# Kernel optimization log

Hardware: AMD Instinct MI355X
Metric: run time of the kernel (lower is better)

The kernel has to match this reference:

```python
import jax, jax.numpy as jnp
import numpy as np

N, E, G, B = 50000, 1600000, 128, 128
FP = 33     # num_feature_pro
ED = 128    # embed_dim
ML = 3000   # max_len


def setup_inputs() -> dict:
    key = jax.random.key(0)
    ks = jax.random.split(key, 20)
    s = lambda k, shape: jax.random.normal(k, shape, jnp.float32) * 0.02
    inp = {}
    inp["pro_x"] = jax.random.normal(ks[0], (N, FP), jnp.float32)
    inp["edge_index"] = jax.random.randint(ks[1], (2, E), 0, N)
    inp["edge_weight"] = jax.random.uniform(ks[2], (E,), jnp.float32)
    inp["pro_batch"] = jnp.sort(jax.random.randint(ks[3], (N,), 0, G))
    inp["rna_global"] = jax.random.randint(ks[4], (B, ML), 0, 5)
    inp["rna_local"] = jax.random.randint(ks[5], (B, ML - 2), 0, 65)
    inp["emb1"] = s(ks[6], (5, ED))
    inp["emb2"] = s(ks[7], (65, ED))
    inp["convW1"] = s(ks[8], (32, ML, 8));     inp["convb1"] = jnp.zeros((32,), jnp.float32)
    inp["convW2"] = s(ks[9], (32, ML - 2, 8)); inp["convb2"] = jnp.zeros((32,), jnp.float32)
    inp["fcxr_W"] = s(ks[10], (32 * 121, 128)); inp["fcxr_b"] = jnp.zeros((128,), jnp.float32)
    inp["gcn1_W"] = s(ks[11], (FP, FP));         inp["gcn1_b"] = jnp.zeros((FP,), jnp.float32)
    inp["gcn2_W"] = s(ks[12], (FP, 2 * FP));     inp["gcn2_b"] = jnp.zeros((2 * FP,), jnp.float32)
    inp["gcn3_W"] = s(ks[13], (2 * FP, 4 * FP)); inp["gcn3_b"] = jnp.zeros((4 * FP,), jnp.float32)
    inp["bn1_g"] = jnp.ones((FP,), jnp.float32);     inp["bn1_b"] = jnp.zeros((FP,), jnp.float32)
    inp["bn2_g"] = jnp.ones((2 * FP,), jnp.float32); inp["bn2_b"] = jnp.zeros((2 * FP,), jnp.float32)
    inp["bn3_g"] = jnp.ones((4 * FP,), jnp.float32); inp["bn3_b"] = jnp.zeros((4 * FP,), jnp.float32)
    inp["fcg1_W"] = s(ks[14], (4 * FP, 1024)); inp["fcg1_b"] = jnp.zeros((1024,), jnp.float32)
    inp["fcg2_W"] = s(ks[15], (1024, 128));    inp["fcg2_b"] = jnp.zeros((128,), jnp.float32)
    return inp


def _gcn(x, W, b, src, dst, ew, n):
    # PyG GCNConv: x' = D^{-1/2}(A+I)D^{-1/2} (x W) + b, self-loop weight 1
    xw = x @ W                                           # [n, out]
    deg = jax.ops.segment_sum(ew, dst, num_segments=n) + 1.0
    dis = jax.lax.rsqrt(deg)
    norm = dis[src] * ew * dis[dst]                      # [E]
    out = jax.ops.segment_sum(xw[src] * norm[:, None], dst, num_segments=n)
    out = out + xw * (dis * dis)[:, None]                # self loops
    return out + b


def _bn(x, g, b, eps=1e-5):
    # NodeLevelBatchNorm (training): batch stats over the node dim, biased var
    m = x.mean(0)
    v = ((x - m) ** 2).mean(0)
    return (x - m) * jax.lax.rsqrt(v + eps) * g + b


def _conv1d(x, W, b):
    # x: [B, C, L], W: [O, C, K] -> [B, O, L-K+1]
    y = jax.lax.conv_general_dilated(x, W, (1,), 'VALID',
                                     dimension_numbers=('NCH', 'OIH', 'NCH'))
    return y + b[None, :, None]


def _rna(tok, emb, cW, cb, fW, fb):
    e = emb[tok]                     # [B, seq, 128] -> channels=seq, length=128
    y = _conv1d(e, cW, cb)           # [B, 32, 121]
    return y.reshape(y.shape[0], -1) @ fW + fb


def reference(pro_x, edge_index, edge_weight, pro_batch, rna_global, rna_local,
              emb1, emb2, convW1, convb1, convW2, convb2, fcxr_W, fcxr_b,
              gcn1_W, gcn1_b, gcn2_W, gcn2_b, gcn3_W, gcn3_b,
              bn1_g, bn1_b, bn2_g, bn2_b, bn3_g, bn3_b,
              fcg1_W, fcg1_b, fcg2_W, fcg2_b):
    src, dst = edge_index[0], edge_index[1]
    n = pro_x.shape[0]
    # RNA branch (fc_xr shared between global and local)
    xrg = _rna(rna_global, emb1, convW1, convb1, fcxr_W, fcxr_b)
    xrl = _rna(rna_local, emb2, convW2, convb2, fcxr_W, fcxr_b)
    # Protein GCN branch
    xp = jax.nn.relu(_bn(_gcn(pro_x, gcn1_W, gcn1_b, src, dst, edge_weight, n), bn1_g, bn1_b))
    ones = jnp.ones_like(edge_weight)
    xp = jax.nn.relu(_bn(_gcn(xp, gcn2_W, gcn2_b, src, dst, ones, n), bn2_g, bn2_b))
    xp = jax.nn.relu(_bn(_gcn(xp, gcn3_W, gcn3_b, src, dst, ones, n), bn3_g, bn3_b))
    # global mean pool per graph
    cnt = jax.ops.segment_sum(jnp.ones((n,), xp.dtype), pro_batch, num_segments=G)
    pooled = jax.ops.segment_sum(xp, pro_batch, num_segments=G) / jnp.maximum(cnt, 1.0)[:, None]
    h = jax.nn.relu(pooled @ fcg1_W + fcg1_b)
    xp_out = h @ fcg2_W + fcg2_b     # dropout = identity (eval)
    xc_rna = (xrg + xrl) * 0.5       # mean over stacked [xrg, xrl]
    return (xc_rna, xp_out)
```

## Files before the change

kernel.cpp:

```cpp
#include <hip/hip_runtime.h>
#include <hip/hip_bf16.h>

typedef __hip_bfloat16 bf16;
typedef unsigned short u16;

#define NN 50000
#define NE 1600000
#define NG 128
#define NB 128
#define SG 3000
#define SL 2998
#define VG 5
#define VL 65
#define EDB 6250
#define AGB 12500
#define NA  (NB*VG + NB*VL)
#define NGB (32*VG + 32*VL)
#define CASTB ((NN*40+255)/256)

__device__ __forceinline__ float b2f(bf16 x){ return __bfloat162float(x); }
__device__ __forceinline__ float blo(unsigned u){ return __uint_as_float(u << 16); }
__device__ __forceinline__ float bhi(unsigned u){ return __uint_as_float(u & 0xffff0000u); }

__device__ void dev_buildG(float (*rows)[128], const float* __restrict__ emb,
                           const float* __restrict__ W, bf16* __restrict__ G,
                           int V, int q){
    int o = q / V, mt = q - o*V;
    int t = threadIdx.x;
    int j = t & 127, half = t >> 7;
    int kk[4], vv[4];
    #pragma unroll
    for (int qq = 0; qq < 4; ++qq){
        int mm = half*4 + qq;
        int m = mt*8 + mm;
        int k = m / V, v = m - k*V;
        kk[qq] = k; vv[qq] = v;
        rows[mm][j] = emb[v*128 + j];
    }
    __syncthreads();
    float a0=0.f, a1=0.f, a2=0.f, a3=0.f;
    const float* Wo = W + o*121*128 + j;
    for (int l = 0; l < 121; ++l){
        float w = Wo[l*128];
        a0 += rows[half*4+0][l + kk[0]] * w;
        a1 += rows[half*4+1][l + kk[1]] * w;
        a2 += rows[half*4+2][l + kk[2]] * w;
        a3 += rows[half*4+3][l + kk[3]] * w;
    }
    float a[4] = {a0, a1, a2, a3};
    #pragma unroll
    for (int qq = 0; qq < 4; ++qq){
        int row = vv[qq]*256 + o*8 + kk[qq];
        G[(size_t)row*128 + j] = __float2bfloat16(a[qq]);
    }
}

__global__ void k_front(const int* __restrict__ rna_g, const int* __restrict__ rna_l,
                        int* __restrict__ tcnt_g, int* __restrict__ toff_g,
                        u16* __restrict__ bucket_g,
                        int* __restrict__ tcnt_l, int* __restrict__ toff_l,
                        u16* __restrict__ bucket_l,
                        const float* __restrict__ convW1, const float* __restrict__ convW2,
                        bf16* __restrict__ Wr1, bf16* __restrict__ Wr2,
                        const float* __restrict__ fcxrW, const float* __restrict__ cb1,
                        const float* __restrict__ cb2, float* __restrict__ bias0,
                        const int* __restrict__ dst, const float* __restrict__ ew,
                        double* __restrict__ packed, int* __restrict__ slot,
                        const float* __restrict__ emb1, const float* __restrict__ emb2,
                        bf16* __restrict__ G1, bf16* __restrict__ G2,
                        const float* __restrict__ pro_x, bf16* __restrict__ xb0){
    __shared__ int hist[VL], pre[VL], cur[VL];
    __shared__ float rows[8][128];
    int bx = blockIdx.x;
    int t = threadIdx.x;
    if (bx < 2*NB){
        int br = bx & 1, b = bx >> 1;
        const int* tok = br ? rna_l : rna_g;
        int S = br ? SL : SG, V = br ? VL : VG;
        int* tcnt = br ? tcnt_l : tcnt_g;
        int* toff = br ? toff_l : toff_g;
        u16* bucket = br ? bucket_l : bucket_g;
        if (t < V) hist[t] = 0;
        __syncthreads();
        for (int i = t; i < S; i += 256) atomicAdd(&hist[tok[b*S + i]], 1);
        __syncthreads();
        if (t == 0){
            int run = 0;
            for (int v = 0; v < V; ++v){ pre[v] = run; run += hist[v]; }
        }
        __syncthreads();
        if (t < V){
            tcnt[b*V + t] = hist[t];
            toff[b*V + t] = pre[t];
            cur[t] = pre[t];
        }
        __syncthreads();
        for (int i = t; i < S; i += 256){
            int v = tok[b*S + i];
            int p = atomicAdd(&cur[v], 1);
            bucket[b*S + p] = (u16)i;
        }
        return;
    }
    bx -= 2*NB;
    if (bx < NGB){
        if (bx < 32*VG) dev_buildG(rows, emb1, fcxrW, G1, VG, bx);
        else dev_buildG(rows, emb2, fcxrW, G2, VL, bx - 32*VG);
        return;
    }
    bx -= NGB;
    if (bx < EDB){
        int e = bx*256 + t;
        double old = unsafeAtomicAdd(&packed[dst[e]], 1048576.0 + (double)ew[e]);
        slot[e] = (int)(old * (1.0/1048576.0));
        return;
    }
    bx -= EDB;
    if (bx < SG + SL){
        const float* W; bf16* Wr; int S, c = bx;
        if (c < SG){ W = convW1; Wr = Wr1; S = SG; }
        else { c -= SG; W = convW2; Wr = Wr2; S = SL; }
        Wr[c*256 + t] = __float2bfloat16(W[((t >> 3)*S + c)*8 + (t & 7)]);
        return;
    }
    bx -= SG + SL;
    if (bx < CASTB){
        int i = bx*256 + t;
        if (i >= NN*40) return;
        int n = i / 40, f = i - n*40;
        xb0[i] = __float2bfloat16(f < 33 ? pro_x[n*33 + f] : 0.f);
        return;
    }
    bx -= CASTB;
    if (t >= 128) return;
    int o = bx, j = t;
    float s = 0.f;
    const float* Wo = fcxrW + o*121*128 + j;
    for (int l = 0; l < 121; ++l) s += Wo[l*128];
    unsafeAtomicAdd(&bias0[j], 0.5f * (cb1[o] + cb2[o]) * s);
}

__device__ void dev_buildA(const bf16* __restrict__ Wr, const u16* __restrict__ bucket,
                           const int* __restrict__ toff, const int* __restrict__ tcnt,
                           float* __restrict__ A, int S, int V, int bv){
    int b = bv / V, v = bv - b*V;
    int t = threadIdx.x;
    const u16* bk = bucket + b*S + toff[b*V + v];
    int m = tcnt[b*V + v];
    float acc = 0.f;
    int idx = 0;
    for (; idx + 4 <= m; idx += 4){
        int c0 = bk[idx], c1 = bk[idx+1], c2 = bk[idx+2], c3 = bk[idx+3];
        acc += b2f(Wr[c0*256 + t]);
        acc += b2f(Wr[c1*256 + t]);
        acc += b2f(Wr[c2*256 + t]);
        acc += b2f(Wr[c3*256 + t]);
    }
    for (; idx < m; ++idx) acc += b2f(Wr[bk[idx]*256 + t]);
    A[b*(256*V) + v*256 + t] = acc;
}

__global__ void k_prep(const double* __restrict__ packed, int* __restrict__ cnt,
                       float2* __restrict__ dis12, float2* __restrict__ self12,
                       const int* __restrict__ batch, int* __restrict__ gstart,
                       int* __restrict__ bsum,
                       const float* __restrict__ fcxrb, const float* __restrict__ bias0,
                       float* __restrict__ out0){
    __shared__ int sd[256];
    int t = threadIdx.x;
    if (blockIdx.x == 49){
        for (int idx = t; idx < NB*128; idx += 256)
            out0[idx] = fcxrb[idx & 127] + bias0[idx & 127];
        return;
    }
    int base = blockIdx.x*1024;
    int s = 0;
    #pragma unroll
    for (int j = 0; j < 4; ++j){
        int i = base + t*4 + j;
        if (i < NN){
            double p = packed[i];
            int c = (int)(p * (1.0/1048576.0));
            float w = (float)(p - (double)c * 1048576.0);
            cnt[i] = c; s += c;
            float r1 = rsqrtf(w + 1.0f);
            float r2 = rsqrtf((float)c + 1.0f);
            dis12[i] = make_float2(r1, r2);
            self12[i] = make_float2(r1*r1, r2*r2);
            int pb = batch[i];
            int prev = (i == 0) ? -1 : batch[i-1];
            for (int g = prev + 1; g <= pb; ++g) gstart[g] = i;
            if (i == NN - 1){
                for (int g = pb + 1; g <= NG; ++g) gstart[g] = NN;
            }
        }
    }
    sd[t] = s; __syncthreads();
    for (int d = 128; d > 0; d >>= 1){
        if (t < d) sd[t] += sd[t+d];
        __syncthreads();
    }
    if (t == 0) bsum[blockIdx.x] = sd[0];
}

__global__ void k_scan3(const int* __restrict__ cnt, const int* __restrict__ bsum,
                        int* __restrict__ offs){
    __shared__ int sd[256];
    __shared__ int sbase;
    int t = threadIdx.x;
    if (t == 0){
        int run = 0;
        for (int i = 0; i < blockIdx.x; ++i) run += bsum[i];
        sbase = run;
    }
    int base = blockIdx.x*1024;
    int loc[4]; int s = 0;
    #pragma unroll
    for (int j = 0; j < 4; ++j){
        int idx = base + t*4 + j;
        loc[j] = (idx < NN) ? cnt[idx] : 0;
        s += loc[j];
    }
    sd[t] = s; __syncthreads();
    for (int d = 1; d < 256; d <<= 1){
        int v = (t >= d) ? sd[t-d] : 0;
        __syncthreads();
        sd[t] += v;
        __syncthreads();
    }
    int run = sbase + (sd[t] - s);
    #pragma unroll
    for (int j = 0; j < 4; ++j){
        int idx = base + t*4 + j;
        if (idx < NN) offs[idx] = run;
        run += loc[j];
    }
}

__global__ void k_F2(const bf16* __restrict__ Wr1, const bf16* __restrict__ Wr2,
                     const u16* __restrict__ bucket_g, const int* __restrict__ toff_g,
                     const int* __restrict__ tcnt_g, float* __restrict__ Ag,
                     const u16* __restrict__ bucket_l, const int* __restrict__ toff_l,
                     const int* __restrict__ tcnt_l, float* __restrict__ Al,
                     const int* __restrict__ src, const int* __restrict__ dst,
                     const float* __restrict__ ew, const float2* __restrict__ dis12,
                     const int* __restrict__ offs, const int* __restrict__ slot,
                     float4* __restrict__ epk){
    int bx = blockIdx.x;
    if (bx < NA){
        if (bx < NB*VG) dev_buildA(Wr1, bucket_g, toff_g, tcnt_g, Ag, SG, VG, bx);
        else dev_buildA(Wr2, bucket_l, toff_l, tcnt_l, Al, SL, VL, bx - NB*VG);
        return;
    }
    int e = (bx - NA)*256 + threadIdx.x;
    int s = src[e], d = dst[e];
    int pos = offs[d] + slot[e];
    float2 a = dis12[s], b = dis12[d];
    float4 v;
    v.x = __int_as_float(s*80);
    v.y = a.x * ew[e] * b.x;
    v.z = a.y * b.y;
    v.w = __int_as_float(s*144);
    epk[pos] = v;
}

template<int QV, int GRP, int OFF_W, int N_Z>
__device__ void dev_agg(float* sAgg ,
                        const bf16* __restrict__ xb, const float4* __restrict__ epk,
                        const int* __restrict__ offs, const int* __restrict__ cnt,
                        const float2* __restrict__ self12,
                        const float* __restrict__ W, const float* __restrict__ bias,
                        float* __restrict__ tout, float* __restrict__ bnpart,
                        int F, int OF, int bx){
    const int LPG = 64 / GRP;
    int wave = threadIdx.x >> 6;
    int node = bx*4 + wave;
    int lane = threadIdx.x & 63;
    int grp  = lane / LPG;
    int gl   = lane % LPG;
    bool act = gl < QV;
    const char* xc = (const char*)xb;
    float a0=0,a1=0,a2=0,a3=0,a4=0,a5=0,a6=0,a7=0;
    int b = offs[node], e = b + cnt[node];
    if (act){
        int fo = gl << 4;
        if (grp == 0){
            float2 sw2 = self12[node];
            float sw = N_Z ? sw2.y : sw2.x;
            uint4 u = *(const uint4*)(xc + node*(QV*16) + fo);
            a0 = sw*blo(u.x); a1 = sw*bhi(u.x); a2 = sw*blo(u.y); a3 = sw*bhi(u.y);
            a4 = sw*blo(u.z); a5 = sw*bhi(u.z); a6 = sw*blo(u.w); a7 = sw*bhi(u.w);
        }
        int p = b + grp;
        for (; p + 3*GRP < e; p += 4*GRP){
            float4 e0 = epk[p];
            float4 e1 = epk[p +   GRP];
            float4 e2 = epk[p + 2*GRP];
            float4 e3 = epk[p + 3*GRP];
            int o0 = __float_as_int(OFF_W ? e0.w : e0.x); float n0 = N_Z ? e0.z : e0.y;
            int o1 = __float_as_int(OFF_W ? e1.w : e1.x); float n1 = N_Z ? e1.z : e1.y;
            int o2 = __float_as_int(OFF_W ? e2.w : e2.x); float n2 = N_Z ? e2.z : e2.y;
            int o3 = __float_as_int(OFF_W ? e3.w : e3.x); float n3 = N_Z ? e3.z : e3.y;
            uint4 u0 = *(const uint4*)(xc + o0 + fo);
            uint4 u1 = *(const uint4*)(xc + o1 + fo);
            uint4 u2 = *(const uint4*)(xc + o2 + fo);
            uint4 u3 = *(const uint4*)(xc + o3 + fo);
            a0 += n0*blo(u0.x); a1 += n0*bhi(u0.x); a2 += n0*blo(u0.y); a3 += n0*bhi(u0.y);
            a4 += n0*blo(u0.z); a5 += n0*bhi(u0.z); a6 += n0*blo(u0.w); a7 += n0*bhi(u0.w);
            a0 += n1*blo(u1.x); a1 += n1*bhi(u1.x); a2 += n1*blo(u1.y); a3 += n1*bhi(u1.y);
            a4 += n1*blo(u1.z); a5 += n1*bhi(u1.z); a6 += n1*blo(u1.w); a7 += n1*bhi(u1.w);
            a0 += n2*blo(u2.x); a1 += n2*bhi(u2.x); a2 += n2*blo(u2.y); a3 += n2*bhi(u2.y);
            a4 += n2*blo(u2.z); a5 += n2*bhi(u2.z); a6 += n2*blo(u2.w); a7 += n2*bhi(u2.w);
            a0 += n3*blo(u3.x); a1 += n3*bhi(u3.x); a2 += n3*blo(u3.y); a3 += n3*bhi(u3.y);
            a4 += n3*blo(u3.z); a5 += n3*bhi(u3.z); a6 += n3*blo(u3.w); a7 += n3*bhi(u3.w);
        }
        if (p < e){
            int p1 = p + GRP, p2 = p + 2*GRP;
            bool v1 = p1 < e, v2 = p2 < e;
            float4 e0 = epk[p];
            float4 e1 = epk[v1 ? p1 : p];
            float4 e2 = epk[v2 ? p2 : p];
            int o0 = __float_as_int(OFF_W ? e0.w : e0.x);
            int o1 = __float_as_int(OFF_W ? e1.w : e1.x);
            int o2 = __float_as_int(OFF_W ? e2.w : e2.x);
            float n0 = N_Z ? e0.z : e0.y;
            float n1 = v1 ? (N_Z ? e1.z : e1.y) : 0.f;
            float n2 = v2 ? (N_Z ? e2.z : e2.y) : 0.f;
            uint4 u0 = *(const uint4*)(xc + o0 + fo);
            uint4 u1 = *(const uint4*)(xc + o1 + fo);
            uint4 u2 = *(const uint4*)(xc + o2 + fo);
            a0 += n0*blo(u0.x); a1 += n0*bhi(u0.x); a2 += n0*blo(u0.y); a3 += n0*bhi(u0.y);
            a4 += n0*blo(u0.z); a5 += n0*bhi(u0.z); a6 += n0*blo(u0.w); a7 += n0*bhi(u0.w);
            a0 += n1*blo(u1.x); a1 += n1*bhi(u1.x); a2 += n1*blo(u1.y); a3 += n1*bhi(u1.y);
            a4 += n1*blo(u1.z); a5 += n1*bhi(u1.z); a6 += n1*blo(u1.w); a7 += n1*bhi(u1.w);
            a0 += n2*blo(u2.x); a1 += n2*bhi(u2.x); a2 += n2*blo(u2.y); a3 += n2*bhi(u2.y);
            a4 += n2*blo(u2.z); a5 += n2*bhi(u2.z); a6 += n2*blo(u2.w); a7 += n2*bhi(u2.w);
        }
    }
    #pragma unroll
    for (int m = LPG; m < 64; m <<= 1){
        a0 += __shfl_xor(a0, m); a1 += __shfl_xor(a1, m);
        a2 += __shfl_xor(a2, m); a3 += __shfl_xor(a3, m);
        a4 += __shfl_xor(a4, m); a5 += __shfl_xor(a5, m);
        a6 += __shfl_xor(a6, m); a7 += __shfl_xor(a7, m);
    }
    if (act && grp == 0){
        float4* dst = (float4*)&sAgg[wave*(QV*8) + gl*8];
        dst[0] = make_float4(a0, a1, a2, a3);
        dst[1] = make_float4(a4, a5, a6, a7);
    }
    __syncthreads();
    int i0 = bx*4;
    int j = threadIdx.x;
    if (j < OF){
        float c0 = bias[j], c1 = c0, c2 = c0, c3 = c0;
        const float* Wj = W + j;
        const float* s0 = sAgg;
        const float* s1 = sAgg + QV*8;
        const float* s2 = sAgg + 2*QV*8;
        const float* s3 = sAgg + 3*QV*8;
        #pragma unroll 4
        for (int f = 0; f < F; ++f){
            float w = Wj[f*OF];
            c0 += s0[f]*w; c1 += s1[f]*w; c2 += s2[f]*w; c3 += s3[f]*w;
        }
        tout[(size_t)(i0+0)*OF + j] = c0;
        tout[(size_t)(i0+1)*OF + j] = c1;
        tout[(size_t)(i0+2)*OF + j] = c2;
        tout[(size_t)(i0+3)*OF + j] = c3;
        float s  = c0 + c1 + c2 + c3;
        float ss = c0*c0 + c1*c1 + c2*c2 + c3*c3;
        float* part = bnpart + (bx & 63)*(2*OF);
        unsafeAtomicAdd(&part[j], s);
        unsafeAtomicAdd(&part[OF + j], ss);
    }
}

template<int QV, int GRP, int OFF_W, int N_Z>
__global__ __launch_bounds__(256, 8)
void k_agg_gemm(const bf16* __restrict__ xb, const float4* __restrict__ epk,
                const int* __restrict__ offs, const int* __restrict__ cnt,
                const float2* __restrict__ self12,
                const float* __restrict__ W, const float* __restrict__ bias,
                float* __restrict__ tout, float* __restrict__ bnpart,
                int F, int OF){
    __shared__ float sAgg[4*QV*8];
    dev_agg<QV,GRP,OFF_W,N_Z>(sAgg, xb, epk, offs, cnt, self12, W, bias,
                              tout, bnpart, F, OF, blockIdx.x);
}

__device__ void dev_gemmR(float* xs , int bq,
                          const float* __restrict__ Ag, const bf16* __restrict__ G1,
                          const float* __restrict__ Al, const bf16* __restrict__ G2,
                          float* __restrict__ out0){
    int kpart = bq >> 4;
    int bgrp  = bq & 15;
    const float* X; const bf16* G; int K, k0;
    if (kpart < 5){ X = Ag; G = G1; K = 1280;  k0 = kpart*256; }
    else          { X = Al; G = G2; K = 16640; k0 = (kpart-5)*256; }
    int b0 = bgrp*8;
    int t = threadIdx.x;
    #pragma unroll
    for (int i = 0; i < 8; ++i)
        xs[i*256 + t] = X[(b0+i)*K + k0 + t];
    __syncthreads();
    int rq = t >> 7, j = t & 127;
    const float* x0 = xs + (rq*4)*256;
    float a0=0,a1=0,a2=0,a3=0;
    const bf16* Gp = G + (size_t)k0*128 + j;
    for (int kk = 0; kk < 256; ++kk){
        float g = b2f(Gp[kk*128]);
        a0 += x0[kk]*g; a1 += x0[256+kk]*g; a2 += x0[512+kk]*g; a3 += x0[768+kk]*g;
    }
    unsafeAtomicAdd(&out0[(b0+rq*4+0)*128 + j], 0.5f*a0);
    unsafeAtomicAdd(&out0[(b0+rq*4+1)*128 + j], 0.5f*a1);
    unsafeAtomicAdd(&out0[(b0+rq*4+2)*128 + j], 0.5f*a2);
    unsafeAtomicAdd(&out0[(b0+rq*4+3)*128 + j], 0.5f*a3);
}

__global__ void k_L3(const bf16* __restrict__ xb, const float4* __restrict__ epk,
                     const int* __restrict__ offs, const int* __restrict__ cnt,
                     const float2* __restrict__ self12,
                     const float* __restrict__ W, const float* __restrict__ bias,
                     float* __restrict__ tout, float* __restrict__ bnpart,
                     const float* __restrict__ Ag, const bf16* __restrict__ G1,
                     const float* __restrict__ Al, const bf16* __restrict__ G2,
                     float* __restrict__ out0){
    __shared__ float smem[8*256];
    int bx = blockIdx.x;
    if (bx < AGB){
        dev_agg<9,4,1,1>(smem, xb, epk, offs, cnt, self12, W, bias, tout, bnpart,
                         66, 132, bx);
    } else {
        dev_gemmR(smem, bx - AGB, Ag, G1, Al, G2, out0);
    }
}

__global__ void k_bn_fin(const float* __restrict__ part, float* __restrict__ sums, int OF){
    int tid = threadIdx.x;
    if (tid >= 2*OF) return;
    float s = 0.f;
    #pragma unroll 8
    for (int k = 0; k < 64; ++k) s += part[k*(2*OF) + tid];
    sums[tid] = s;
}

__global__ void k_bn_apply(const float* __restrict__ t, const float* __restrict__ sums,
                           const float* __restrict__ g, const float* __restrict__ b,
                           bf16* __restrict__ xo, int OF, int OS, int total){
    int id = blockIdx.x*256 + threadIdx.x;
    if (id >= total) return;
    int i = id / OS, f = id - i*OS;
    float v = 0.f;
    if (f < OF){
        float m  = sums[f] * (1.0f/(float)NN);
        float vr = sums[OF + f] * (1.0f/(float)NN) - m*m;
        float sc = g[f] * rsqrtf(vr + 1e-5f);
        float sh = b[f] - m*sc;
        v = t[(size_t)i*OF + f] * sc + sh;
        v = v > 0.f ? v : 0.f;
    }
    xo[id] = __float2bfloat16(v);
}

__global__ void k_fcgF(const float* __restrict__ bufB, const float* __restrict__ sums,
                       const float* __restrict__ bn3g, const float* __restrict__ bn3b,
                       const int* __restrict__ gstart,
                       const float* __restrict__ W1, const float* __restrict__ b1,
                       const float* __restrict__ W2, const float* __restrict__ b2,
                       float* __restrict__ out){
    __shared__ float scs[132], shs[132];
    __shared__ float pp[7][132];
    __shared__ float pr[132];
    __shared__ float hr[1024];
    __shared__ float part[8][128];
    int g = blockIdx.x, t = threadIdx.x;
    if (t < 132){
        float m  = sums[t] * (1.0f/(float)NN);
        float vr = sums[132 + t] * (1.0f/(float)NN) - m*m;
        float sc = bn3g[t] * rsqrtf(vr + 1e-5f);
        scs[t] = sc;
        shs[t] = bn3b[t] - m*sc;
    }
    __syncthreads();
    int i0 = gstart[g], i1 = gstart[g+1];
    int r = t / 132, f = t - r*132;
    if (r < 7){
        float acc = 0.f;
        for (int i = i0 + r; i < i1; i += 7){
            float v = bufB[(size_t)i*132 + f] * scs[f] + shs[f];
            acc += v > 0.f ? v : 0.f;
        }
        pp[r][f] = acc;
    }
    __syncthreads();
    if (t < 132){
        float s = 0.f;
        #pragma unroll
        for (int k = 0; k < 7; ++k) s += pp[k][t];
        float inv = 1.0f / fmaxf((float)(i1 - i0), 1.0f);
        pr[t] = s * inv;
    }
    __syncthreads();
    float acc = b1[t];
    #pragma unroll 4
    for (int ff = 0; ff < 132; ++ff) acc += pr[ff] * W1[ff*1024 + t];
    hr[t] = acc > 0.f ? acc : 0.f;
    __syncthreads();
    int ks = t >> 7, j = t & 127;
    const float* Wp = W2 + (ks*128)*128 + j;
    const float* hp = hr + ks*128;
    float a = 0.f;
    #pragma unroll 8
    for (int kk = 0; kk < 128; ++kk) a += hp[kk] * Wp[(size_t)kk*128];
    part[ks][j] = a;
    __syncthreads();
    if (t < 128){
        float s = b2[t];
        #pragma unroll
        for (int rr = 0; rr < 8; ++rr) s += part[rr][t];
        out[g*128 + t] = s;
    }
}

extern "C" void kernel_launch(void* const* d_in, const int* in_sizes, int n_in,
                              void* d_out, int out_size, void* d_ws, size_t ws_size,
                              hipStream_t stream)
{
    (void)in_sizes; (void)n_in; (void)out_size; (void)ws_size;

    const float* pro_x  = (const float*)d_in[0];
    const int*   eidx   = (const int*)  d_in[1];
    const float* ew     = (const float*)d_in[2];
    const int*   pbatch = (const int*)  d_in[3];
    const int*   rna_g  = (const int*)  d_in[4];
    const int*   rna_l  = (const int*)  d_in[5];
    const float* emb1   = (const float*)d_in[6];
    const float* emb2   = (const float*)d_in[7];
    const float* convW1 = (const float*)d_in[8];
    const float* convb1 = (const float*)d_in[9];
    const float* convW2 = (const float*)d_in[10];
    const float* convb2 = (const float*)d_in[11];
    const float* fcxrW  = (const float*)d_in[12];
    const float* fcxrb  = (const float*)d_in[13];
    const float* g1W = (const float*)d_in[14];
    const float* g1b = (const float*)d_in[15];
    const float* g2W = (const float*)d_in[16];
    const float* g2b = (const float*)d_in[17];
    const float* g3W = (const float*)d_in[18];
    const float* g3b = (const float*)d_in[19];
    const float* bn1g = (const float*)d_in[20];
    const float* bn1b = (const float*)d_in[21];
    const float* bn2g = (const float*)d_in[22];
    const float* bn2b = (const float*)d_in[23];
    const float* bn3g = (const float*)d_in[24];
    const float* bn3b = (const float*)d_in[25];
    const float* fcg1W = (const float*)d_in[26];
    const float* fcg1b = (const float*)d_in[27];
    const float* fcg2W = (const float*)d_in[28];
    const float* fcg2b = (const float*)d_in[29];

    const int* e_src = eidx;
    const int* e_dst = eidx + NE;

    char* base = (char*)d_ws;
    size_t off = 0;
    auto alloc = [&](size_t bytes)->char*{
        off = (off + 255) & ~(size_t)255;
        char* p = base + off; off += bytes; return p;
    };

    double* packed  = (double*)alloc(NN*8);
    float* bnsum1  = (float*)alloc(2*33*4);
    float* bnsum2  = (float*)alloc(2*66*4);
    float* bnsum3  = (float*)alloc(2*132*4);
    float* bias0   = (float*)alloc(128*4);
    float* bnpart1 = (float*)alloc(64*2*33*4);
    float* bnpart2 = (float*)alloc(64*2*66*4);
    float* bnpart3 = (float*)alloc(64*2*132*4);
    size_t zero_bytes = (off + 255) & ~(size_t)255;

    int*    cnt    = (int*)   alloc(NN*4);
    float2* dis12  = (float2*)alloc(NN*8);
    float2* self12 = (float2*)alloc(NN*8);
    int*    offs   = (int*)   alloc(NN*4);
    int*    bsum   = (int*)   alloc(64*4);
    int*    gstart = (int*)   alloc((NG+1)*4);
    float4* epk    = (float4*)alloc((size_t)NE*16);
    float*  bufB   = (float*) alloc((size_t)NN*132*4);
    bf16*   xbA    = (bf16*)  alloc((size_t)NE*4);
    bf16*   xbB    = (bf16*)  alloc((size_t)NN*72*2);
    float*  Ag     = (float*) alloc((size_t)NB*256*VG*4);
    float*  Al     = (float*) alloc((size_t)NB*256*VL*4);
    bf16*   G1     = (bf16*)  alloc((size_t)32*8*VG*128*2);
    bf16*   G2     = (bf16*)  alloc((size_t)32*8*VL*128*2);

    int*  slot = (int*)xbA;
    bf16* xb0  = (bf16*)xbB;

    float* out0 = (float*)d_out;
    float* out1 = (float*)d_out + 16384;

    char* rb = (char*)bufB;
    size_t ro = 0;
    auto ralloc = [&](size_t bytes)->char*{
        ro = (ro + 255) & ~(size_t)255;
        char* p = rb + ro; ro += bytes; return p;
    };
    int* toff_g   = (int*)ralloc(NB*VG*4);
    int* toff_l   = (int*)ralloc(NB*VL*4);
    int* tcnt_g   = (int*)ralloc(NB*VG*4);
    int* tcnt_l   = (int*)ralloc(NB*VL*4);
    u16* bucket_g = (u16*)ralloc((size_t)NB*SG*2);
    u16* bucket_l = (u16*)ralloc((size_t)NB*SL*2);
    bf16* Wr1     = (bf16*)ralloc((size_t)SG*256*2);
    bf16* Wr2     = (bf16*)ralloc((size_t)SL*256*2);

    hipMemsetAsync(d_ws, 0, zero_bytes, stream);

    k_front<<<2*NB + NGB + EDB + SG + SL + CASTB + 32, 256, 0, stream>>>(
        rna_g, rna_l, tcnt_g, toff_g, bucket_g, tcnt_l, toff_l, bucket_l,
        convW1, convW2, Wr1, Wr2, fcxrW, convb1, convb2, bias0,
        e_dst, ew, packed, slot,
        emb1, emb2, G1, G2, pro_x, xb0);

    k_prep<<<50, 256, 0, stream>>>(packed, cnt, dis12, self12, pbatch, gstart,
                                   bsum, fcxrb, bias0, out0);
    k_scan3<<<49, 256, 0, stream>>>(cnt, bsum, offs);

    k_F2<<<NA + EDB, 256, 0, stream>>>(Wr1, Wr2,
                                       bucket_g, toff_g, tcnt_g, Ag,
                                       bucket_l, toff_l, tcnt_l, Al,
                                       e_src, e_dst, ew, dis12, offs, slot, epk);

    k_agg_gemm<5,8,0,0><<<AGB, 256, 0, stream>>>(xb0, epk, offs, cnt, self12,
                                                 g1W, g1b, bufB, bnpart1, 33, 33);
    k_bn_fin<<<1, 512, 0, stream>>>(bnpart1, bnsum1, 33);
    k_bn_apply<<<(NN*40+255)/256, 256, 0, stream>>>(bufB, bnsum1, bn1g, bn1b,
                                                    xbA, 33, 40, NN*40);

    k_agg_gemm<5,8,0,1><<<AGB, 256, 0, stream>>>(xbA, epk, offs, cnt, self12,
                                                 g2W, g2b, bufB, bnpart2, 33, 66);
    k_bn_fin<<<1, 512, 0, stream>>>(bnpart2, bnsum2, 66);
    k_bn_apply<<<(NN*72+255)/256, 256, 0, stream>>>(bufB, bnsum2, bn2g, bn2b,
                                                    xbB, 66, 72, NN*72);

    k_L3<<<AGB + 1120, 256, 0, stream>>>(xbB, epk, offs, cnt, self12,
                                         g3W, g3b, bufB, bnpart3, Ag, G1, Al, G2, out0);
    k_bn_fin<<<1, 512, 0, stream>>>(bnpart3, bnsum3, 132);

    k_fcgF<<<NG, 1024, 0, stream>>>(bufB, bnsum3, bn3g, bn3b, gstart,
                                    fcg1W, fcg1b, fcg2W, fcg2b, out1);
}
```

Baseline: 567.7 us.

## Move RNA GEMM blocks into layer-2 kernel and unroll bucket gather by eight

The RNA output GEMM blocks are moved out of the layer-3 aggregation launch and into a new fused layer-2 kernel, where they are scheduled first, ahead of the aggregation blocks. Layer 3 now runs only aggregation blocks and uses a much smaller shared-memory array, which may allow more resident blocks. The buildA gather loop is unrolled to eight loads with a tree reduction for more memory-level parallelism. The risk is that the GEMM blocks now compete with layer-2 aggregation instead of layer-3, and the smaller smem in k_L3 must be enough for dev_agg<9,4,1,1>.

```diff
diff --git a/kernel.cpp b/kernel.cpp
--- a/kernel.cpp
+++ b/kernel.cpp
@@ -17,6 +17,7 @@
 #define NA  (NB*VG + NB*VL)
 #define NGB (32*VG + 32*VL)
 #define CASTB ((NN*40+255)/256)
+#define NGR 1120
 
 __device__ __forceinline__ float b2f(bf16 x){ return __bfloat162float(x); }
 __device__ __forceinline__ float blo(unsigned u){ return __uint_as_float(u << 16); }
@@ -149,12 +150,18 @@
     int m = tcnt[b*V + v];
     float acc = 0.f;
     int idx = 0;
-    for (; idx + 4 <= m; idx += 4){
-        int c0 = bk[idx], c1 = bk[idx+1], c2 = bk[idx+2], c3 = bk[idx+3];
-        acc += b2f(Wr[c0*256 + t]);
-        acc += b2f(Wr[c1*256 + t]);
-        acc += b2f(Wr[c2*256 + t]);
-        acc += b2f(Wr[c3*256 + t]);
+    for (; idx + 8 <= m; idx += 8){
+        int c0 = bk[idx  ], c1 = bk[idx+1], c2 = bk[idx+2], c3 = bk[idx+3];
+        int c4 = bk[idx+4], c5 = bk[idx+5], c6 = bk[idx+6], c7 = bk[idx+7];
+        float s0 = b2f(Wr[c0*256 + t]);
+        float s1 = b2f(Wr[c1*256 + t]);
+        float s2 = b2f(Wr[c2*256 + t]);
+        float s3 = b2f(Wr[c3*256 + t]);
+        float s4 = b2f(Wr[c4*256 + t]);
+        float s5 = b2f(Wr[c5*256 + t]);
+        float s6 = b2f(Wr[c6*256 + t]);
+        float s7 = b2f(Wr[c7*256 + t]);
+        acc += ((s0 + s1) + (s2 + s3)) + ((s4 + s5) + (s6 + s7));
     }
     for (; idx < m; ++idx) acc += b2f(Wr[bk[idx]*256 + t]);
     A[b*(256*V) + v*256 + t] = acc;
@@ -418,7 +425,7 @@
     unsafeAtomicAdd(&out0[(b0+rq*4+3)*128 + j], 0.5f*a3);
 }
 
-__global__ void k_L3(const bf16* __restrict__ xb, const float4* __restrict__ epk,
+__global__ void k_L2(const bf16* __restrict__ xb, const float4* __restrict__ epk,
                      const int* __restrict__ offs, const int* __restrict__ cnt,
                      const float2* __restrict__ self12,
                      const float* __restrict__ W, const float* __restrict__ bias,
@@ -428,12 +435,22 @@
                      float* __restrict__ out0){
     __shared__ float smem[8*256];
     int bx = blockIdx.x;
-    if (bx < AGB){
-        dev_agg<9,4,1,1>(smem, xb, epk, offs, cnt, self12, W, bias, tout, bnpart,
-                         66, 132, bx);
+    if (bx < NGR){
+        dev_gemmR(smem, bx, Ag, G1, Al, G2, out0);
     } else {
-        dev_gemmR(smem, bx - AGB, Ag, G1, Al, G2, out0);
-    }
+        dev_agg<5,8,0,1>(smem, xb, epk, offs, cnt, self12, W, bias, tout, bnpart,
+                         33, 66, bx - NGR);
+    }
+}
+
+__global__ void k_L3(const bf16* __restrict__ xb, const float4* __restrict__ epk,
+                     const int* __restrict__ offs, const int* __restrict__ cnt,
+                     const float2* __restrict__ self12,
+                     const float* __restrict__ W, const float* __restrict__ bias,
+                     float* __restrict__ tout, float* __restrict__ bnpart){
+    __shared__ float smem[4*9*8];
+    dev_agg<9,4,1,1>(smem, xb, epk, offs, cnt, self12, W, bias, tout, bnpart,
+                     66, 132, blockIdx.x);
 }
 
 __global__ void k_bn_fin(const float* __restrict__ part, float* __restrict__ sums, int OF){
@@ -639,14 +656,15 @@
     k_bn_apply<<<(NN*40+255)/256, 256, 0, stream>>>(bufB, bnsum1, bn1g, bn1b,
                                                     xbA, 33, 40, NN*40);
 
-    k_agg_gemm<5,8,0,1><<<AGB, 256, 0, stream>>>(xbA, epk, offs, cnt, self12,
-                                                 g2W, g2b, bufB, bnpart2, 33, 66);
+    k_L2<<<NGR + AGB, 256, 0, stream>>>(xbA, epk, offs, cnt, self12,
+                                        g2W, g2b, bufB, bnpart2,
+                                        Ag, G1, Al, G2, out0);
     k_bn_fin<<<1, 512, 0, stream>>>(bnpart2, bnsum2, 66);
     k_bn_apply<<<(NN*72+255)/256, 256, 0, stream>>>(bufB, bnsum2, bn2g, bn2b,
                                                     xbB, 66, 72, NN*72);
 
-    k_L3<<<AGB + 1120, 256, 0, stream>>>(xbB, epk, offs, cnt, self12,
-                                         g3W, g3b, bufB, bnpart3, Ag, G1, Al, G2, out0);
+    k_L3<<<AGB, 256, 0, stream>>>(xbB, epk, offs, cnt, self12,
+                                  g3W, g3b, bufB, bnpart3);
     k_bn_fin<<<1, 512, 0, stream>>>(bnpart3, bnsum3, 132);
 
     k_fcgF<<<NG, 1024, 0, stream>>>(bufB, bnsum3, bn3g, bn3b, gstart,
```

After: 571.4 us. No clear change (+0.7%).
